# Performance work log

Hardware: AMD Instinct MI355X
Metric: run time of the kernel (lower is better)

The kernel has to match this reference:

```python
import jax, jax.numpy as jnp
import numpy as np

SIGMA = 1.0          # from global `args.sigma` in the original repo
ALPHA = 0.99         # self.alpha
TOPK = 4             # torch.topk(W, 4)
NUM_CLASSES = 2
EPS = float(np.finfo(float).eps)


def setup_inputs() -> dict:
    key = jax.random.key(0)
    k1, k2, k3 = jax.random.split(key, 3)
    labeled_inputs = jax.random.normal(k1, (1024, 1024), dtype=jnp.float32)
    labeled_target = jax.random.randint(k2, (1024,), 0, NUM_CLASSES, dtype=jnp.int64)
    unlabeled_inputs = jax.random.normal(k3, (3072, 1024), dtype=jnp.float32)
    return {"labeled_inputs": labeled_inputs,
            "labeled_target": labeled_target,
            "unlabeled_inputs": unlabeled_inputs}


def _label_prop(labeled_inputs, unlabeled_inputs, labeled_target):
    num_support = labeled_inputs.shape[0]
    emb_all = jnp.concatenate([labeled_inputs, unlabeled_inputs], axis=0)  # [N, d]
    N, d = emb_all.shape

    # mean_j (x_i - x_k)_j^2 = (|x_i|^2 + |x_k|^2 - 2 x_i.x_k) / d
    # (algebraically identical to the torch NxNxd broadcast, without materializing it)
    sq = jnp.sum(emb_all * emb_all, axis=1)                 # [N]
    dist = (sq[:, None] + sq[None, :] - 2.0 * (emb_all @ emb_all.T)) / d
    W = jnp.exp(-dist / (2.0 * SIGMA * SIGMA))              # [N, N]

    # zero the diagonal
    eye = jnp.eye(N, dtype=W.dtype)
    W = W * (1.0 - eye)

    # top-k per row -> symmetric binary mask
    _, indices = jax.lax.top_k(W, TOPK)                     # [N, k]
    mask = jnp.zeros_like(W)
    rows = jnp.arange(N)[:, None]
    mask = mask.at[rows, indices].set(1.0)
    mask = ((mask + mask.T) > 0).astype(jnp.float32)
    W = W * mask

    # symmetric degree normalization S = D^{-1/2} W D^{-1/2}
    D = W.sum(axis=0)                                       # [N]
    D_sqrt_inv = jnp.sqrt(1.0 / (D + EPS))
    S = D_sqrt_inv[:, None] * W * D_sqrt_inv[None, :]

    # labels: one-hot support, zeros for queries
    ys = jax.nn.one_hot(labeled_target, NUM_CLASSES, dtype=jnp.float32)
    yu = jnp.zeros((N - num_support, NUM_CLASSES), dtype=jnp.float32)
    y = jnp.concatenate([ys, yu], axis=0)                   # [N, C]

    # F = (I - alpha*S + eps)^{-1} y   (solve == inverse @ y)
    A = jnp.eye(N, dtype=jnp.float32) - ALPHA * S + EPS
    Fk = jnp.linalg.solve(A, y)
    return Fk[num_support:, :]                              # [num_queries, C]


def reference(labeled_inputs, labeled_target, unlabeled_inputs):
    return _label_prop(labeled_inputs, unlabeled_inputs, labeled_target)
```

## Files before the change

### kernel.cpp

```cpp
#include <hip/hip_runtime.h>

#define N_ALL 4096
#define N_LAB 1024
#define DIMF 1024
#define EDGECAP 32768
#define ALPHA_ 0.99f
#define NIT_CH 100
#define EPS_D 2.220446049250313e-16

typedef short bf16x8 __attribute__((ext_vector_type(8)));
typedef float f32x4 __attribute__((ext_vector_type(4)));

struct __align__(8) Edge { unsigned j; float w; };

__device__ inline const float* xrow(const float* L, const float* U, int r) {
  return (r < N_LAB) ? (L + (size_t)r * DIMF) : (U + (size_t)(r - N_LAB) * DIMF);
}

__device__ inline void load_lds16(const void* g, void* l) {
  __builtin_amdgcn_global_load_lds(
      (const __attribute__((address_space(1))) unsigned int*)g,
      (__attribute__((address_space(3))) unsigned int*)l, 16, 0, 0);
}

__device__ inline unsigned short bf16rne(float f) {
  unsigned u = __float_as_uint(f);
  unsigned r = (u + 0x7fffu + ((u >> 16) & 1u)) >> 16;
  return (unsigned short)r;
}

__global__ __launch_bounds__(256) void labfmt_k(const int* __restrict__ lab,
                                                int* __restrict__ flag) {
  const long long* l64 = (const long long*)lab;
  int bad = 0;
  for (int k = threadIdx.x; k < 512; k += 256) {
    long long v = l64[k];
    if (v != 0 && v != 1) bad = 1;
  }
  __shared__ int sbad[4];
  unsigned long long m = __ballot(bad);
  if ((threadIdx.x & 63) == 0) sbad[threadIdx.x >> 6] = (m != 0ull);
  __syncthreads();
  if (threadIdx.x == 0)
    flag[0] = (sbad[0] | sbad[1] | sbad[2] | sbad[3]) ? 0 : 1;
}

__global__ __launch_bounds__(256) void prep_k(const float* __restrict__ L,
                                              const float* __restrict__ U,
                                              unsigned short* __restrict__ Xbf,
                                              float* __restrict__ sq,
                                              double* __restrict__ sqd) {
  const int row = blockIdx.x;
  const int tid = threadIdx.x;
  const float* src = xrow(L, U, row);
  float4 v = ((const float4*)src)[tid];
  ushort4 h;
  h.x = bf16rne(v.x); h.y = bf16rne(v.y); h.z = bf16rne(v.z); h.w = bf16rne(v.w);
  ((ushort4*)(Xbf + (size_t)row * DIMF))[tid] = h;
  float s = v.x * v.x + v.y * v.y + v.z * v.z + v.w * v.w;
  double sd = (double)v.x * v.x + (double)v.y * v.y +
              (double)v.z * v.z + (double)v.w * v.w;
#pragma unroll
  for (int d = 32; d >= 1; d >>= 1) {
    s += __shfl_xor(s, d);
    sd += __shfl_xor(sd, d);
  }
  __shared__ float wsum[4];
  __shared__ double wsumd[4];
  if ((tid & 63) == 0) { wsum[tid >> 6] = s; wsumd[tid >> 6] = sd; }
  __syncthreads();
  if (tid == 0) {
    sq[row] = wsum[0] + wsum[1] + wsum[2] + wsum[3];
    sqd[row] = wsumd[0] + wsumd[1] + wsumd[2] + wsumd[3];
  }
}

__global__ __launch_bounds__(256) void gemm_w(const unsigned short* __restrict__ Xbf,
                                              const float* __restrict__ sq,
                                              float* __restrict__ W) {
  __shared__ unsigned short At[128 * 32];
  __shared__ unsigned short Bt[128 * 32];
  const int tid = threadIdx.x;
  const int wave = tid >> 6, lane = tid & 63;
  const int brow = blockIdx.y * 128, bcol = blockIdx.x * 128;
  const int q = lane >> 4, rl = lane & 15;
  const int wr = (wave >> 1) * 64, wc = (wave & 1) * 64;

  f32x4 acc[4][4] = {};

  const int srow = tid >> 2;
  const int soff = (tid & 3) * 8;

  for (int k0 = 0; k0 < DIMF; k0 += 32) {
#pragma unroll
    for (int half = 0; half < 2; ++half) {
      const unsigned short* ga =
          Xbf + (size_t)(brow + half * 64 + srow) * DIMF + k0 + soff;
      load_lds16(ga, &At[(half * 64 + wave * 16) * 32]);
      const unsigned short* gb =
          Xbf + (size_t)(bcol + half * 64 + srow) * DIMF + k0 + soff;
      load_lds16(gb, &Bt[(half * 64 + wave * 16) * 32]);
    }
    __syncthreads();
    bf16x8 af[4], bf_[4];
#pragma unroll
    for (int t = 0; t < 4; ++t) {
      af[t] = *(const bf16x8*)&At[(wr + t * 16 + rl) * 32 + q * 8];
      bf_[t] = *(const bf16x8*)&Bt[(wc + t * 16 + rl) * 32 + q * 8];
    }
#pragma unroll
    for (int i = 0; i < 4; ++i)
#pragma unroll
      for (int j = 0; j < 4; ++j)
        acc[i][j] = __builtin_amdgcn_mfma_f32_16x16x32_bf16(af[i], bf_[j], acc[i][j], 0, 0, 0);
    __syncthreads();
  }

#pragma unroll
  for (int i = 0; i < 4; ++i) {
#pragma unroll
    for (int j = 0; j < 4; ++j) {
#pragma unroll
      for (int reg = 0; reg < 4; ++reg) {
        int gr = brow + wr + i * 16 + q * 4 + reg;
        int gc = bcol + wc + j * 16 + rl;
        float g = acc[i][j][reg];
        float dist = (sq[gr] + sq[gc] - 2.0f * g) * (1.0f / 1024.0f);
        float w = expf(-0.5f * dist);
        if (gr == gc) w = 0.0f;
        W[(size_t)gr * N_ALL + gc] = w;
      }
    }
  }
}

__global__ __launch_bounds__(256) void top8_k(const float* __restrict__ W,
                                              unsigned* __restrict__ t8i) {
  const int wave = threadIdx.x >> 6, lane = threadIdx.x & 63;
  const int row = blockIdx.x * 4 + wave;
  const float* Wr = W + (size_t)row * N_ALL;
  float bv[8]; unsigned bj[8];
#pragma unroll
  for (int t = 0; t < 8; ++t) { bv[t] = -1.0f; bj[t] = 0xFFFFFFFFu; }
  float minv = -1.0f; int mins = 0;
  for (int s = 0; s < 64; ++s) {
    int j = s * 64 + lane;
    float v = Wr[j];
    if (v > minv) {
#pragma unroll
      for (int t = 0; t < 8; ++t) if (t == mins) { bv[t] = v; bj[t] = (unsigned)j; }
      minv = bv[0]; mins = 0;
#pragma unroll
      for (int t = 1; t < 8; ++t) if (bv[t] < minv) { minv = bv[t]; mins = t; }
    }
  }
  for (int pick = 0; pick < 8; ++pick) {
    unsigned long long best = 0;
#pragma unroll
    for (int t = 0; t < 8; ++t) {
      bool valid = (bv[t] >= 0.0f);
      unsigned long long key =
          ((unsigned long long)__float_as_uint(bv[t]) << 32) |
          (unsigned long long)(0xFFFFFFFFu - bj[t]);
      if (valid && key > best) best = key;
    }
#pragma unroll
    for (int d = 32; d >= 1; d >>= 1) {
      unsigned long long o = __shfl_xor(best, d);
      if (o > best) best = o;
    }
    unsigned wj = 0xFFFFFFFFu - (unsigned)(best & 0xFFFFFFFFull);
    if (lane == 0) t8i[row * 8 + pick] = wj;
#pragma unroll
    for (int t = 0; t < 8; ++t) if (bj[t] == wj) bv[t] = -1.0f;
  }
}

__global__ __launch_bounds__(256) void rerank_k(const float* __restrict__ L,
                                                const float* __restrict__ U,
                                                const double* __restrict__ sqd,
                                                const unsigned* __restrict__ t8i,
                                                unsigned* __restrict__ t4i) {
  const int wave = threadIdx.x >> 6, lane = threadIdx.x & 63;
  const int row = blockIdx.x * 4 + wave;
  const float* xi = xrow(L, U, row);
  float xr[16];
#pragma unroll
  for (int t = 0; t < 16; ++t) xr[t] = xi[t * 64 + lane];
  unsigned cj[8];
  double cw[8];
#pragma unroll
  for (int c = 0; c < 8; ++c) cj[c] = t8i[row * 8 + c];
  for (int c = 0; c < 8; ++c) {
    const float* xj = xrow(L, U, (int)cj[c]);
    double s = 0.0;
#pragma unroll
    for (int t = 0; t < 16; ++t) s += (double)xr[t] * xj[t * 64 + lane];
#pragma unroll
    for (int d = 32; d >= 1; d >>= 1) s += __shfl_xor(s, d);
    double dist = (sqd[row] + sqd[cj[c]] - 2.0 * s) * (1.0 / 1024.0);
    cw[c] = exp(-0.5 * dist);
  }
  if (lane == 0) {
#pragma unroll
    for (int pick = 0; pick < 4; ++pick) {
      int ms = -1;
      double mv = -1.0;
      unsigned mj = 0xFFFFFFFFu;
#pragma unroll
      for (int c = 0; c < 8; ++c) {
        bool better = (cw[c] > mv) || (cw[c] == mv && cj[c] < mj);
        if (cw[c] >= 0.0 && better) { mv = cw[c]; mj = cj[c]; ms = c; }
      }
      t4i[row * 4 + pick] = mj;
      cw[ms] = -2.0;
    }
  }
}

__global__ __launch_bounds__(256) void cnt4_k(const unsigned* __restrict__ t4i,
                                              unsigned* __restrict__ nn) {
  const int wave = threadIdx.x >> 6, lane = threadIdx.x & 63;
  const int i = blockIdx.x * 4 + wave;
  const uint4 mine = ((const uint4*)t4i)[i];
  unsigned base = 0;
  for (int j0 = 0; j0 < N_ALL; j0 += 64) {
    int j = j0 + lane;
    uint4 tj = ((const uint4*)t4i)[j];
    bool keep = (mine.x == (unsigned)j) | (mine.y == (unsigned)j) |
                (mine.z == (unsigned)j) | (mine.w == (unsigned)j) |
                (tj.x == (unsigned)i) | (tj.y == (unsigned)i) |
                (tj.z == (unsigned)i) | (tj.w == (unsigned)i);
    keep = keep && (j != i);
    base += (unsigned)__popcll(__ballot(keep));
  }
  if (lane == 0) nn[i] = base;
}

__global__ __launch_bounds__(64) void scanP_k(const unsigned* __restrict__ nn,
                                              unsigned* __restrict__ rowPtr) {
  const int lane = threadIdx.x;
  unsigned running = 0;
  for (int j0 = 0; j0 < N_ALL; j0 += 64) {
    int v = (int)nn[j0 + lane];
    int incl = v;
#pragma unroll
    for (int d = 1; d < 64; d <<= 1) {
      int t = __shfl_up(incl, d);
      if (lane >= d) incl += t;
    }
    rowPtr[j0 + lane] = running + (unsigned)(incl - v);
    running += (unsigned)__shfl(incl, 63);
  }
  if (lane == 0) rowPtr[N_ALL] = running;
}

__global__ __launch_bounds__(256) void csrfill_k(const unsigned* __restrict__ t4i,
                                                 const unsigned* __restrict__ rowPtr,
                                                 Edge* __restrict__ edges,
                                                 unsigned* __restrict__ eRow) {
  const int wave = threadIdx.x >> 6, lane = threadIdx.x & 63;
  const int i = blockIdx.x * 4 + wave;
  const uint4 mine = ((const uint4*)t4i)[i];
  unsigned base = rowPtr[i];
  for (int j0 = 0; j0 < N_ALL; j0 += 64) {
    int j = j0 + lane;
    uint4 tj = ((const uint4*)t4i)[j];
    bool keep = (mine.x == (unsigned)j) | (mine.y == (unsigned)j) |
                (mine.z == (unsigned)j) | (mine.w == (unsigned)j) |
                (tj.x == (unsigned)i) | (tj.y == (unsigned)i) |
                (tj.z == (unsigned)i) | (tj.w == (unsigned)i);
    keep = keep && (j != i);
    unsigned long long m = __ballot(keep);
    if (keep) {
      unsigned pos = base + (unsigned)__popcll(m & ((1ull << lane) - 1ull));
      edges[pos].j = (unsigned)j;
      edges[pos].w = 0.0f;
      eRow[pos] = (unsigned)i;
    }
    base += (unsigned)__popcll(m);
  }
}

__global__ __launch_bounds__(256) void edgeval_k(const float* __restrict__ L,
                                                 const float* __restrict__ U,
                                                 const double* __restrict__ sqd,
                                                 const unsigned* __restrict__ rowPtr,
                                                 const unsigned* __restrict__ eRow,
                                                 Edge* __restrict__ edges) {
  const int wave = threadIdx.x >> 6, lane = threadIdx.x & 63;
  const unsigned e = blockIdx.x * 4 + wave;
  if (e >= rowPtr[N_ALL]) return;
  const unsigned i = eRow[e];
  const unsigned j = edges[e].j;
  const float* xi = xrow(L, U, (int)i);
  const float* xj = xrow(L, U, (int)j);
  double s = 0.0;
#pragma unroll
  for (int t = 0; t < 16; ++t)
    s += (double)xi[t * 64 + lane] * xj[t * 64 + lane];
#pragma unroll
  for (int d = 32; d >= 1; d >>= 1) s += __shfl_xor(s, d);
  if (lane == 0) {
    double dist = (sqd[i] + sqd[j] - 2.0 * s) * (1.0 / 1024.0);
    edges[e].w = (float)exp(-0.5 * dist);
  }
}

__global__ __launch_bounds__(256) void degE_k(const unsigned* __restrict__ rowPtr,
                                              const Edge* __restrict__ edges,
                                              float* __restrict__ Dis) {
  const int wave = threadIdx.x >> 6, lane = threadIdx.x & 63;
  const int i = blockIdx.x * 4 + wave;
  const unsigned b0 = rowPtr[i], b1 = rowPtr[i + 1];
  double ds = 0.0;
  for (unsigned e = b0 + lane; e < b1; e += 64) ds += (double)edges[e].w;
#pragma unroll
  for (int d = 32; d >= 1; d >>= 1) ds += __shfl_xor(ds, d);
  if (lane == 0) Dis[i] = (float)sqrt(1.0 / (ds + EPS_D));
}

__global__ __launch_bounds__(256) void scaleE_k(const unsigned* __restrict__ rowPtr,
                                                const unsigned* __restrict__ eRow,
                                                const float* __restrict__ Dis,
                                                Edge* __restrict__ edges) {
  const unsigned e = blockIdx.x * 256 + threadIdx.x;
  if (e >= rowPtr[N_ALL]) return;
  Edge ed = edges[e];
  edges[e].w = ed.w * Dis[eRow[e]] * Dis[ed.j];
}

__global__ __launch_bounds__(256) void init_k(const int* __restrict__ lab,
                                              const int* __restrict__ labflag,
                                              float2* __restrict__ x,
                                              float2* __restrict__ r,
                                              float2* __restrict__ d) {
  const int m = blockIdx.x * 256 + threadIdx.x;
  const int isI64 = labflag[0];
  float2 b = make_float2(0.0f, 0.0f);
  if (m < N_LAB) {
    int c = isI64 ? lab[2 * m] : lab[m];
    b.x = (c == 0) ? 1.0f : 0.0f;
    b.y = (c == 1) ? 1.0f : 0.0f;
  }
  x[m] = make_float2(0.0f, 0.0f);
  r[m] = b;
  d[m] = b;
}

__global__ __launch_bounds__(512) void chebit_k(const Edge* __restrict__ edges,
                                                const unsigned* __restrict__ rowPtr,
                                                const float2* __restrict__ dIn,
                                                float2* __restrict__ dOut,
                                                float2* __restrict__ x,
                                                float2* __restrict__ r,
                                                float c1, float c2, int last) {
  const int row = blockIdx.x * 8 + (threadIdx.x >> 6);
  const int lane = threadIdx.x & 63;
  const unsigned b0 = rowPtr[row], b1 = rowPtr[row + 1];
  float ax = 0.0f, ay = 0.0f;
  for (unsigned e = b0 + lane; e < b1; e += 64) {
    Edge ed = edges[e];
    float2 dj = dIn[ed.j];
    ax += ed.w * dj.x;
    ay += ed.w * dj.y;
  }
#pragma unroll
  for (int d = 32; d >= 1; d >>= 1) {
    ax += __shfl_xor(ax, d);
    ay += __shfl_xor(ay, d);
  }
  if (lane == 0) {
    float2 di = dIn[row], xi = x[row], ri = r[row];
    xi.x += di.x; xi.y += di.y;
    ri.x += ALPHA_ * ax - di.x;
    ri.y += ALPHA_ * ay - di.y;
    x[row] = xi;
    r[row] = ri;
    if (!last) {
      float2 dn;
      dn.x = c1 * di.x + c2 * ri.x;
      dn.y = c1 * di.y + c2 * ri.y;
      dOut[row] = dn;
    }
  }
}

__global__ __launch_bounds__(256) void out_k(const float2* __restrict__ x,
                                             float2* __restrict__ out) {
  const int q = blockIdx.x * 256 + threadIdx.x;
  out[q] = x[N_LAB + q];
}

extern "C" void kernel_launch(void* const* d_in, const int* in_sizes, int n_in,
                              void* d_out, int out_size, void* d_ws, size_t ws_size,
                              hipStream_t stream) {
  int iL = 0, iT = 1, iU = 2;
  for (int i = 0; i < n_in; ++i) {
    if (in_sizes[i] == N_LAB * DIMF) iL = i;
    else if (in_sizes[i] == (N_ALL - N_LAB) * DIMF) iU = i;
    else iT = i;
  }
  const float* L = (const float*)d_in[iL];
  const int* lab = (const int*)d_in[iT];
  const float* U = (const float*)d_in[iU];
  float2* out = (float2*)d_out;

  char* w = (char*)d_ws;
  size_t off = 0;
  auto alloc = [&](size_t bytes) {
    void* p = (void*)(w + off);
    off += (bytes + 255) & ~(size_t)255;
    return p;
  };
  float* W = (float*)alloc((size_t)N_ALL * N_ALL * 4);
  unsigned short* Xbf = (unsigned short*)alloc((size_t)N_ALL * DIMF * 2);
  float* sq = (float*)alloc(N_ALL * 4);
  double* sqd = (double*)alloc(N_ALL * 8);
  unsigned* t8i = (unsigned*)alloc(N_ALL * 8 * 4);
  unsigned* t4i = (unsigned*)alloc(N_ALL * 4 * 4);
  float* Dis = (float*)alloc(N_ALL * 4);
  unsigned* nn = (unsigned*)alloc(N_ALL * 4);
  unsigned* rowPtr = (unsigned*)alloc((N_ALL + 1) * 4);
  int* labflag = (int*)alloc(256);
  Edge* edges = (Edge*)alloc((size_t)EDGECAP * sizeof(Edge));
  unsigned* eRow = (unsigned*)alloc((size_t)EDGECAP * 4);
  float2* xv = (float2*)alloc(N_ALL * 8);
  float2* rv = (float2*)alloc(N_ALL * 8);
  float2* dv0 = (float2*)alloc(N_ALL * 8);
  float2* dv1 = (float2*)alloc(N_ALL * 8);
  if (off > ws_size) return;

  labfmt_k<<<1, 256, 0, stream>>>(lab, labflag);
  prep_k<<<N_ALL, 256, 0, stream>>>(L, U, Xbf, sq, sqd);
  gemm_w<<<dim3(32, 32), 256, 0, stream>>>(Xbf, sq, W);
  top8_k<<<N_ALL / 4, 256, 0, stream>>>(W, t8i);
  rerank_k<<<N_ALL / 4, 256, 0, stream>>>(L, U, sqd, t8i, t4i);
  cnt4_k<<<N_ALL / 4, 256, 0, stream>>>(t4i, nn);
  scanP_k<<<1, 64, 0, stream>>>(nn, rowPtr);
  csrfill_k<<<N_ALL / 4, 256, 0, stream>>>(t4i, rowPtr, edges, eRow);
  edgeval_k<<<EDGECAP / 4, 256, 0, stream>>>(L, U, sqd, rowPtr, eRow, edges);
  degE_k<<<N_ALL / 4, 256, 0, stream>>>(rowPtr, edges, Dis);
  scaleE_k<<<EDGECAP / 256, 256, 0, stream>>>(rowPtr, eRow, Dis, edges);
  init_k<<<N_ALL / 256, 256, 0, stream>>>(lab, labflag, xv, rv, dv0);

  const double theta = 1.0, delta = 0.992;
  const double sigma1 = theta / delta;
  double rho = delta / theta;
  float2* dA = dv0;
  float2* dB = dv1;
  for (int k = 0; k < NIT_CH; ++k) {
    const int last = (k == NIT_CH - 1);
    const double rho_new = 1.0 / (2.0 * sigma1 - rho);
    const float c1 = (float)(rho_new * rho);
    const float c2 = (float)(2.0 * rho_new / delta);
    chebit_k<<<N_ALL / 8, 512, 0, stream>>>(edges, rowPtr, dA, dB, xv, rv,
                                            c1, c2, last);
    rho = rho_new;
    float2* t = dA; dA = dB; dB = t;
  }
  out_k<<<(N_ALL - N_LAB) / 256, 256, 0, stream>>>(xv, out);
}
```

Measured before the change: 647.3 us.

## Fuse Chebyshev iterations into a single-block persistent kernel with LDS vectors

Replaces the 100 per-iteration chebit launches, plus the init and output kernels, with one 1024-thread block that keeps the iterate vectors in registers and the search direction in shared memory. Edges are repacked into a transposed, strided layout (32 slots per thread) with 16-bit indices. Each thread accumulates segmented row sums and flushes them through LDS atomics. This removes the per-iteration kernel launch and global-memory round trips, at the cost of running on a single CU, performing 32 serial edge loads per thread per iteration, and assuming the edge count fits within EDGECAP.

```diff
diff --git a/kernel.cpp b/kernel.cpp
--- a/kernel.cpp
+++ b/kernel.cpp
@@ -330,66 +330,113 @@
   edges[e].w = ed.w * Dis[eRow[e]] * Dis[ed.j];
 }
 
-__global__ __launch_bounds__(256) void init_k(const int* __restrict__ lab,
-                                              const int* __restrict__ labflag,
-                                              float2* __restrict__ x,
-                                              float2* __restrict__ r,
-                                              float2* __restrict__ d) {
-  const int m = blockIdx.x * 256 + threadIdx.x;
+__global__ __launch_bounds__(256) void repack_k(const Edge* __restrict__ edges,
+                                                const unsigned* __restrict__ eRow,
+                                                const unsigned* __restrict__ rowPtr,
+                                                unsigned short* __restrict__ jT,
+                                                float* __restrict__ wT,
+                                                unsigned short* __restrict__ rowT) {
+  const unsigned pos = blockIdx.x * 256 + threadIdx.x;
+  const unsigned nnz = rowPtr[N_ALL];
+  const unsigned slot = (pos & 31) * 1024 + (pos >> 5);
+  if (pos < nnz) {
+    jT[slot] = (unsigned short)edges[pos].j;
+    wT[slot] = edges[pos].w;
+    rowT[slot] = (unsigned short)eRow[pos];
+  } else {
+    jT[slot] = 0;
+    wT[slot] = 0.0f;
+    rowT[slot] = 0;
+  }
+}
+
+__global__ __launch_bounds__(1024) void cheb_solve(const int* __restrict__ lab,
+                                                   const int* __restrict__ labflag,
+                                                   const unsigned short* __restrict__ jT,
+                                                   const float* __restrict__ wT,
+                                                   const unsigned short* __restrict__ rowT,
+                                                   float2* __restrict__ out) {
+  __shared__ float2 dS[N_ALL];
+  __shared__ float2 acc[N_ALL];
+  const int tid = threadIdx.x;
   const int isI64 = labflag[0];
-  float2 b = make_float2(0.0f, 0.0f);
-  if (m < N_LAB) {
-    int c = isI64 ? lab[2 * m] : lab[m];
-    b.x = (c == 0) ? 1.0f : 0.0f;
-    b.y = (c == 1) ? 1.0f : 0.0f;
-  }
-  x[m] = make_float2(0.0f, 0.0f);
-  r[m] = b;
-  d[m] = b;
-}
-
-__global__ __launch_bounds__(512) void chebit_k(const Edge* __restrict__ edges,
-                                                const unsigned* __restrict__ rowPtr,
-                                                const float2* __restrict__ dIn,
-                                                float2* __restrict__ dOut,
-                                                float2* __restrict__ x,
-                                                float2* __restrict__ r,
-                                                float c1, float c2, int last) {
-  const int row = blockIdx.x * 8 + (threadIdx.x >> 6);
-  const int lane = threadIdx.x & 63;
-  const unsigned b0 = rowPtr[row], b1 = rowPtr[row + 1];
-  float ax = 0.0f, ay = 0.0f;
-  for (unsigned e = b0 + lane; e < b1; e += 64) {
-    Edge ed = edges[e];
-    float2 dj = dIn[ed.j];
-    ax += ed.w * dj.x;
-    ay += ed.w * dj.y;
-  }
-#pragma unroll
-  for (int d = 32; d >= 1; d >>= 1) {
-    ax += __shfl_xor(ax, d);
-    ay += __shfl_xor(ay, d);
-  }
-  if (lane == 0) {
-    float2 di = dIn[row], xi = x[row], ri = r[row];
-    xi.x += di.x; xi.y += di.y;
-    ri.x += ALPHA_ * ax - di.x;
-    ri.y += ALPHA_ * ay - di.y;
-    x[row] = xi;
-    r[row] = ri;
-    if (!last) {
-      float2 dn;
-      dn.x = c1 * di.x + c2 * ri.x;
-      dn.y = c1 * di.y + c2 * ri.y;
-      dOut[row] = dn;
-    }
-  }
-}
-
-__global__ __launch_bounds__(256) void out_k(const float2* __restrict__ x,
-                                             float2* __restrict__ out) {
-  const int q = blockIdx.x * 256 + threadIdx.x;
-  out[q] = x[N_LAB + q];
+  float2 x[4], rv[4], dv[4];
+#pragma unroll
+  for (int u = 0; u < 4; ++u) {
+    int m = tid + u * 1024;
+    float2 b = make_float2(0.0f, 0.0f);
+    if (m < N_LAB) {
+      int c = isI64 ? lab[2 * m] : lab[m];
+      b.x = (c == 0) ? 1.0f : 0.0f;
+      b.y = (c == 1) ? 1.0f : 0.0f;
+    }
+    x[u] = make_float2(0.0f, 0.0f);
+    rv[u] = b;
+    dv[u] = b;
+    dS[m] = b;
+    acc[m] = make_float2(0.0f, 0.0f);
+  }
+  int prevRow = (int)rowT[tid];
+  const int r0 = prevRow;
+  unsigned mask = 0;
+#pragma unroll
+  for (int k = 1; k < 32; ++k) {
+    int rw = (int)rowT[k * 1024 + tid];
+    if (rw != prevRow) mask |= 1u << (k - 1);
+    prevRow = rw;
+  }
+  mask |= 1u << 31;
+  __syncthreads();
+
+  const double theta = 1.0, delta = 0.992;
+  const double sigma1 = theta / delta;
+  double rho = delta / theta;
+  for (int it = 0;; ++it) {
+    float ax = 0.0f, ay = 0.0f;
+    int fl = 0;
+#pragma unroll
+    for (int k = 0; k < 32; ++k) {
+      const int idx = k * 1024 + tid;
+      float wv = wT[idx];
+      int j = (int)jT[idx];
+      float2 dj = dS[j];
+      ax += wv * dj.x;
+      ay += wv * dj.y;
+      if ((mask >> k) & 1u) {
+        atomicAdd(&acc[r0 + fl].x, ax);
+        atomicAdd(&acc[r0 + fl].y, ay);
+        ax = 0.0f; ay = 0.0f;
+        ++fl;
+      }
+    }
+    __syncthreads();
+    const bool last = (it == NIT_CH - 1);
+    const double rho_new = 1.0 / (2.0 * sigma1 - rho);
+    const float c1 = (float)(rho_new * rho);
+    const float c2 = (float)(2.0 * rho_new / delta);
+    rho = rho_new;
+#pragma unroll
+    for (int u = 0; u < 4; ++u) {
+      int m = tid + u * 1024;
+      float2 a = acc[m];
+      acc[m] = make_float2(0.0f, 0.0f);
+      x[u].x += dv[u].x; x[u].y += dv[u].y;
+      rv[u].x += ALPHA_ * a.x - dv[u].x;
+      rv[u].y += ALPHA_ * a.y - dv[u].y;
+      if (!last) {
+        dv[u].x = c1 * dv[u].x + c2 * rv[u].x;
+        dv[u].y = c1 * dv[u].y + c2 * rv[u].y;
+        dS[m] = dv[u];
+      }
+    }
+    if (last) break;
+    __syncthreads();
+  }
+#pragma unroll
+  for (int u = 1; u < 4; ++u) {
+    int m = tid + u * 1024;
+    out[m - N_LAB] = x[u];
+  }
 }
 
 extern "C" void kernel_launch(void* const* d_in, const int* in_sizes, int n_in,
@@ -425,10 +472,9 @@
   int* labflag = (int*)alloc(256);
   Edge* edges = (Edge*)alloc((size_t)EDGECAP * sizeof(Edge));
   unsigned* eRow = (unsigned*)alloc((size_t)EDGECAP * 4);
-  float2* xv = (float2*)alloc(N_ALL * 8);
-  float2* rv = (float2*)alloc(N_ALL * 8);
-  float2* dv0 = (float2*)alloc(N_ALL * 8);
-  float2* dv1 = (float2*)alloc(N_ALL * 8);
+  unsigned short* jT = (unsigned short*)alloc((size_t)EDGECAP * 2);
+  float* wT = (float*)alloc((size_t)EDGECAP * 4);
+  unsigned short* rowT = (unsigned short*)alloc((size_t)EDGECAP * 2);
   if (off > ws_size) return;
 
   labfmt_k<<<1, 256, 0, stream>>>(lab, labflag);
@@ -442,22 +488,6 @@
   edgeval_k<<<EDGECAP / 4, 256, 0, stream>>>(L, U, sqd, rowPtr, eRow, edges);
   degE_k<<<N_ALL / 4, 256, 0, stream>>>(rowPtr, edges, Dis);
   scaleE_k<<<EDGECAP / 256, 256, 0, stream>>>(rowPtr, eRow, Dis, edges);
-  init_k<<<N_ALL / 256, 256, 0, stream>>>(lab, labflag, xv, rv, dv0);
-
-  const double theta = 1.0, delta = 0.992;
-  const double sigma1 = theta / delta;
-  double rho = delta / theta;
-  float2* dA = dv0;
-  float2* dB = dv1;
-  for (int k = 0; k < NIT_CH; ++k) {
-    const int last = (k == NIT_CH - 1);
-    const double rho_new = 1.0 / (2.0 * sigma1 - rho);
-    const float c1 = (float)(rho_new * rho);
-    const float c2 = (float)(2.0 * rho_new / delta);
-    chebit_k<<<N_ALL / 8, 512, 0, stream>>>(edges, rowPtr, dA, dB, xv, rv,
-                                            c1, c2, last);
-    rho = rho_new;
-    float2* t = dA; dA = dB; dB = t;
-  }
-  out_k<<<(N_ALL - N_LAB) / 256, 256, 0, stream>>>(xv, out);
-}
+  repack_k<<<EDGECAP / 256, 256, 0, stream>>>(edges, eRow, rowPtr, jT, wT, rowT);
+  cheb_solve<<<1, 1024, 0, stream>>>(lab, labflag, jT, wT, rowT, out);
+}
```

New measurement: 1.776 ms. +174.4%, slower.
